# Kernel optimization log

Measured on AMD Instinct MI355X. Metric: run time of the kernel, lower is better.

Reference implementation:

```python
import jax, jax.numpy as jnp
import numpy as np

MAGNITUDE = 9
PROB = 0.5
WARP_STRENGTH = MAGNITUDE * 0.3 / 9.0  # = 0.3


def _notaknot_matrix(S):
    # System for second derivatives M of a cubic spline on uniform grid h=1
    # (scipy CubicSpline default bc_type='not-a-knot').
    A = np.zeros((S, S), dtype=np.float32)
    i = np.arange(1, S - 1)
    A[i, i - 1] = 1.0
    A[i, i] = 4.0
    A[i, i + 1] = 1.0
    # not-a-knot: third derivative continuous at x1 and x_{S-2}
    A[0, 0], A[0, 1], A[0, 2] = 1.0, -2.0, 1.0
    A[-1, -3], A[-1, -2], A[-1, -1] = 1.0, -2.0, 1.0
    return A


def setup_inputs() -> dict:
    key = jax.random.key(0)
    k1, k2, k3 = jax.random.split(key, 3)
    B, C, S = 128, 64, 4096
    x = jax.random.normal(k1, (B, C, S), dtype=jnp.float32)
    # per-sample scale ~ U(1 - warp_strength, 1 + warp_strength)
    scale = (1.0 - WARP_STRENGTH) + 2.0 * WARP_STRENGTH * jax.random.uniform(k2, (B,), dtype=jnp.float32)
    # per-sample apply decision: rand < prob
    apply_mask = jax.random.uniform(k3, (B,)) < PROB
    return {"x": x, "scale": scale, "apply_mask": apply_mask}


def reference(x, scale, apply_mask):
    B, C, S = x.shape
    A = jnp.asarray(_notaknot_matrix(S))  # (S, S), fixed uniform-grid system

    # --- fit not-a-knot cubic splines for all B*C signals at once ---
    y = x.reshape(B * C, S)
    rhs = jnp.zeros_like(y).at[:, 1:-1].set(
        6.0 * (y[:, :-2] - 2.0 * y[:, 1:-1] + y[:, 2:])
    )  # not-a-knot rows have rhs 0
    M = jnp.linalg.solve(A, rhs.T).T.reshape(B, C, S)  # second derivatives

    # --- warped evaluation points (shared across channels of a sample) ---
    grid = jnp.arange(S, dtype=x.dtype)
    w = jnp.clip(grid[None, :] * scale[:, None], 0.0, S - 1)  # (B, S)
    idx = jnp.clip(jnp.floor(w).astype(jnp.int32), 0, S - 2)  # interval index
    t = (w - idx.astype(x.dtype))[:, None, :]                 # (B, 1, S)

    idx3 = jnp.broadcast_to(idx[:, None, :], (B, C, S))
    y0 = jnp.take_along_axis(x, idx3, axis=2)
    y1 = jnp.take_along_axis(x, idx3 + 1, axis=2)
    M0 = jnp.take_along_axis(M, idx3, axis=2)
    M1 = jnp.take_along_axis(M, idx3 + 1, axis=2)

    # s(t) = y0 + b t + c t^2 + d t^3 on each unit interval (h = 1)
    b = (y1 - y0) - (2.0 * M0 + M1) / 6.0
    c = M0 / 2.0
    d = (M1 - M0) / 6.0
    warped = y0 + t * (b + t * (c + t * d))

    return jnp.where(apply_mask[:, None, None], warped, x)
```

## Files before the change

kernel.cpp:

```cpp
#include <hip/hip_runtime.h>
#include <math.h>


#define SLEN 4096
#define WRAD 8
#define BLK  256
#define NG   4

__global__ __launch_bounds__(BLK, 3) void time_warp_kernel(
    const float* __restrict__ x,
    const float* __restrict__ scale,
    const int*   __restrict__ apply_mask,
    float* __restrict__ out,
    int C)
{
    __shared__ float sy[SLEN];
    __shared__ float sf[SLEN + 2 * WRAD];
    __shared__ float sm[SLEN];

    const int bid = blockIdx.x;
    const int b   = bid / C;
    const int t   = threadIdx.x;
    const float* __restrict__ xin = x   + (size_t)bid * SLEN;
    float*       __restrict__ o   = out + (size_t)bid * SLEN;

    if (apply_mask[b] == 0) {
        const float4* __restrict__ xi4 = (const float4*)xin;
        float4*       __restrict__ o4  = (float4*)o;
        #pragma unroll
        for (int s = 0; s < NG; ++s)
            o4[t + BLK * s] = xi4[t + BLK * s];
        return;
    }

    {
        const float4* __restrict__ xi4 = (const float4*)xin;
        #pragma unroll
        for (int s = 0; s < NG; ++s)
            *(float4*)&sy[4 * t + 1024 * s] = xi4[t + BLK * s];
    }
    if (t < WRAD)                      sf[t] = 0.0f;
    else if (t >= 16 && t < 16 + WRAD) sf[(SLEN + 2 * WRAD - 1) - (t - 16)] = 0.0f;
    __syncthreads();

    const float M1  = sy[0]        - 2.0f * sy[1]        + sy[2];
    const float MS2 = sy[SLEN - 3] - 2.0f * sy[SLEN - 2] + sy[SLEN - 1];

    #pragma unroll
    for (int s = 0; s < NG; ++s) {
        const int j0 = 4 * t + 1024 * s;
        float4 yc = *(const float4*)&sy[j0];
        float  ym = (j0 > 0)        ? sy[j0 - 1] : 0.0f;
        float  yp = (j0 + 4 < SLEN) ? sy[j0 + 4] : 0.0f;
        float yv[6] = {ym, yc.x, yc.y, yc.z, yc.w, yp};
        float fe[4];
        #pragma unroll
        for (int e = 0; e < 4; ++e) {
            const int j = j0 + e;
            float v = 6.0f * (yv[e] - 2.0f * yv[e + 1] + yv[e + 2]);
            if (j < 2 || j > SLEN - 3) v = 0.0f;
            if (j == 2)        v -= M1;
            if (j == SLEN - 3) v -= MS2;
            fe[e] = v;
        }
        *(float4*)&sf[WRAD + j0] = make_float4(fe[0], fe[1], fe[2], fe[3]);
    }
    __syncthreads();

    const float r = 0.26794919243112270f;
    float G[WRAD + 1];
    G[0] = 0.28867513459481287f;
    #pragma unroll
    for (int k = 1; k <= WRAD; ++k) G[k] = -G[k - 1] * r;
    const float log2r = -1.8999686269529532f;

    float v1 = 0.0f, vS2 = 0.0f;
    #pragma unroll
    for (int k = 1; k <= WRAD; ++k) {
        v1  += G[k] * sf[WRAD + 1 + k];
        vS2 += G[k] * sf[WRAD + (SLEN - 2) - k];
    }

    #pragma unroll
    for (int s = 0; s < NG; ++s) {
        const int j0 = 4 * t + 1024 * s;
        float fw[4 * (WRAD / 4) * 2 + 4];
        #pragma unroll
        for (int m = 0; m < 5; ++m)
            *(float4*)&fw[4 * m] = *(const float4*)&sf[j0 + 4 * m];
        float mv[4];
        #pragma unroll
        for (int e = 0; e < 4; ++e) {
            float acc = G[0] * fw[WRAD + e];
            #pragma unroll
            for (int k = 1; k <= WRAD; ++k)
                acc += G[k] * (fw[WRAD + e - k] + fw[WRAD + e + k]);
            const int i = j0 + e;
            if (i >= 2 && i <= 34) {
                float cc = v1 * exp2f((float)(i - 1) * log2r);
                acc += (i & 1) ? -cc : cc;
            }
            if (i >= SLEN - 36 && i <= SLEN - 3) {
                float cc = vS2 * exp2f((float)(SLEN - 2 - i) * log2r);
                acc += (i & 1) ? cc : -cc;
            }
            mv[e] = acc;
        }
        if (j0 == 0)        { mv[1] = M1;  mv[0] = 2.0f * M1  - mv[2]; }
        if (j0 == SLEN - 4) { mv[2] = MS2; mv[3] = 2.0f * MS2 - mv[1]; }
        *(float4*)&sm[j0] = make_float4(mv[0], mv[1], mv[2], mv[3]);
    }
    __syncthreads();

    const float sc = scale[b];
    #pragma unroll
    for (int s = 0; s < NG; ++s) {
        const int j0 = 4 * t + 1024 * s;
        float rv[4];
        #pragma unroll
        for (int e = 0; e < 4; ++e) {
            const int j = j0 + e;
            float w = fminf((float)j * sc, (float)(SLEN - 1));
            int idx = (int)w;
            if (idx > SLEN - 2) idx = SLEN - 2;
            float tt  = w - (float)idx;
            float y0  = sy[idx];
            float y1  = sy[idx + 1];
            float m0  = sm[idx];
            float m1v = sm[idx + 1];
            float bb = (y1 - y0) - (2.0f * m0 + m1v) * (1.0f / 6.0f);
            float cc = 0.5f * m0;
            float dd = (m1v - m0) * (1.0f / 6.0f);
            rv[e] = y0 + tt * (bb + tt * (cc + tt * dd));
        }
        ((float4*)o)[t + BLK * s] = make_float4(rv[0], rv[1], rv[2], rv[3]);
    }
}

extern "C" void kernel_launch(void* const* d_in, const int* in_sizes, int n_in,
                              void* d_out, int out_size, void* d_ws, size_t ws_size,
                              hipStream_t stream) {
    const float* x     = (const float*)d_in[0];
    const float* scale = (const float*)d_in[1];
    const int*   mask  = (const int*)d_in[2];
    float*       out   = (float*)d_out;

    const int B     = in_sizes[1];
    const int total = in_sizes[0];
    const int C     = total / (B * SLEN);
    const int nblk  = B * C;

    time_warp_kernel<<<nblk, BLK, 0, stream>>>(x, scale, mask, out, C);
}
```

Before: 230.5 us.

## Fold second-difference RHS into filter taps, drop sf buffer and one barrier

The rhs stencil is folded algebraically into the truncated inverse filter, giving combined taps H applied directly to the signal. This removes the intermediate shared rhs array and one __syncthreads, with explicit corrections applied only near the boundaries. The smaller shared footprint allows launch bounds of 4 blocks per CU. The final evaluation now writes scalar coalesced stores per thread instead of float4 groups, which changes the LDS gather pattern and risks some precision differences from the truncated 7-tap filter.

```diff
diff --git a/kernel.cpp b/kernel.cpp
--- a/kernel.cpp
+++ b/kernel.cpp
@@ -3,11 +3,10 @@
 
 
 #define SLEN 4096
-#define WRAD 8
 #define BLK  256
 #define NG   4
 
-__global__ __launch_bounds__(BLK, 3) void time_warp_kernel(
+__global__ __launch_bounds__(BLK, 4) void time_warp_kernel(
     const float* __restrict__ x,
     const float* __restrict__ scale,
     const int*   __restrict__ apply_mask,
@@ -15,7 +14,6 @@
     int C)
 {
     __shared__ float sy[SLEN];
-    __shared__ float sf[SLEN + 2 * WRAD];
     __shared__ float sm[SLEN];
 
     const int bid = blockIdx.x;
@@ -39,101 +37,115 @@
         for (int s = 0; s < NG; ++s)
             *(float4*)&sy[4 * t + 1024 * s] = xi4[t + BLK * s];
     }
-    if (t < WRAD)                      sf[t] = 0.0f;
-    else if (t >= 16 && t < 16 + WRAD) sf[(SLEN + 2 * WRAD - 1) - (t - 16)] = 0.0f;
     __syncthreads();
 
-    const float M1  = sy[0]        - 2.0f * sy[1]        + sy[2];
-    const float MS2 = sy[SLEN - 3] - 2.0f * sy[SLEN - 2] + sy[SLEN - 1];
+    const float log2r = -1.8999686269529532f;
+    float Gt[10];
+    Gt[0] = 0.28867513459481287f;
+    #pragma unroll
+    for (int k = 1; k <= 7; ++k) Gt[k] = -Gt[k - 1] * 0.26794919243112270f;
+    Gt[8] = 0.0f; Gt[9] = 0.0f;
+    float H[9];
+    H[0] = 6.0f * (2.0f * Gt[1] - 2.0f * Gt[0]);
+    #pragma unroll
+    for (int k = 1; k <= 8; ++k) H[k] = 6.0f * (Gt[k - 1] - 2.0f * Gt[k] + Gt[k + 1]);
+
+    auto gax = [&](int d) -> float {
+        int a = d < 0 ? -d : d;
+        if (a > 7) return 0.0f;
+        float g = 0.28867513459481287f * exp2f((float)a * log2r);
+        return (a & 1) ? -g : g;
+    };
 
     #pragma unroll
     for (int s = 0; s < NG; ++s) {
         const int j0 = 4 * t + 1024 * s;
-        float4 yc = *(const float4*)&sy[j0];
-        float  ym = (j0 > 0)        ? sy[j0 - 1] : 0.0f;
-        float  yp = (j0 + 4 < SLEN) ? sy[j0 + 4] : 0.0f;
-        float yv[6] = {ym, yc.x, yc.y, yc.z, yc.w, yp};
-        float fe[4];
-        #pragma unroll
-        for (int e = 0; e < 4; ++e) {
-            const int j = j0 + e;
-            float v = 6.0f * (yv[e] - 2.0f * yv[e + 1] + yv[e + 2]);
-            if (j < 2 || j > SLEN - 3) v = 0.0f;
-            if (j == 2)        v -= M1;
-            if (j == SLEN - 3) v -= MS2;
-            fe[e] = v;
+        float fw[20];
+        if (j0 >= 8 && j0 <= SLEN - 12) {
+            #pragma unroll
+            for (int m = 0; m < 5; ++m)
+                *(float4*)&fw[4 * m] = *(const float4*)&sy[j0 - 8 + 4 * m];
+        } else {
+            #pragma unroll
+            for (int m = 0; m < 20; ++m) {
+                int yi = j0 - 8 + m;
+                int yc = yi < 0 ? 0 : (yi > SLEN - 1 ? SLEN - 1 : yi);
+                float v = sy[yc];
+                fw[m] = (yi < 0 || yi > SLEN - 1) ? 0.0f : v;
+            }
         }
-        *(float4*)&sf[WRAD + j0] = make_float4(fe[0], fe[1], fe[2], fe[3]);
-    }
-    __syncthreads();
-
-    const float r = 0.26794919243112270f;
-    float G[WRAD + 1];
-    G[0] = 0.28867513459481287f;
-    #pragma unroll
-    for (int k = 1; k <= WRAD; ++k) G[k] = -G[k - 1] * r;
-    const float log2r = -1.8999686269529532f;
-
-    float v1 = 0.0f, vS2 = 0.0f;
-    #pragma unroll
-    for (int k = 1; k <= WRAD; ++k) {
-        v1  += G[k] * sf[WRAD + 1 + k];
-        vS2 += G[k] * sf[WRAD + (SLEN - 2) - k];
-    }
-
-    #pragma unroll
-    for (int s = 0; s < NG; ++s) {
-        const int j0 = 4 * t + 1024 * s;
-        float fw[4 * (WRAD / 4) * 2 + 4];
-        #pragma unroll
-        for (int m = 0; m < 5; ++m)
-            *(float4*)&fw[4 * m] = *(const float4*)&sf[j0 + 4 * m];
         float mv[4];
         #pragma unroll
         for (int e = 0; e < 4; ++e) {
-            float acc = G[0] * fw[WRAD + e];
+            float acc = H[0] * fw[8 + e];
             #pragma unroll
-            for (int k = 1; k <= WRAD; ++k)
-                acc += G[k] * (fw[WRAD + e - k] + fw[WRAD + e + k]);
-            const int i = j0 + e;
-            if (i >= 2 && i <= 34) {
-                float cc = v1 * exp2f((float)(i - 1) * log2r);
-                acc += (i & 1) ? -cc : cc;
-            }
-            if (i >= SLEN - 36 && i <= SLEN - 3) {
-                float cc = vS2 * exp2f((float)(SLEN - 2 - i) * log2r);
-                acc += (i & 1) ? cc : -cc;
-            }
+            for (int k = 1; k <= 8; ++k)
+                acc += H[k] * (fw[8 + e - k] + fw[8 + e + k]);
             mv[e] = acc;
         }
-        if (j0 == 0)        { mv[1] = M1;  mv[0] = 2.0f * M1  - mv[2]; }
-        if (j0 == SLEN - 4) { mv[2] = MS2; mv[3] = 2.0f * MS2 - mv[1]; }
+
+        if (j0 <= 12) {
+            float M1v  = sy[0] - 2.0f * sy[1] + sy[2];
+            float fspm = 6.0f * sy[0];
+            float fsp0 = 6.0f * (sy[1] - 2.0f * sy[0]);
+            float fsp1 = 6.0f * M1v;
+            float v1 = 0.0f;
+            #pragma unroll
+            for (int k = 1; k <= 7; ++k)
+                v1 += Gt[k] * 6.0f * (sy[k] - 2.0f * sy[k + 1] + sy[k + 2]);
+            v1 -= Gt[1] * M1v;
+            #pragma unroll
+            for (int e = 0; e < 4; ++e) {
+                int i = j0 + e;
+                float corr = gax(i + 1) * fspm + gax(i) * fsp0
+                           + gax(i - 1) * fsp1 + gax(i - 2) * M1v;
+                float img = v1 * exp2f((float)(i - 1) * log2r);
+                mv[e] = mv[e] - corr + ((i & 1) ? -img : img);
+            }
+            if (j0 == 0) { mv[1] = M1v; mv[0] = 2.0f * M1v - mv[2]; }
+        }
+        if (j0 >= SLEN - 16) {
+            float MS2v = sy[SLEN - 3] - 2.0f * sy[SLEN - 2] + sy[SLEN - 1];
+            float fspA = 6.0f * MS2v;
+            float fspB = 6.0f * (sy[SLEN - 2] - 2.0f * sy[SLEN - 1]);
+            float fspC = 6.0f * sy[SLEN - 1];
+            float vS2 = 0.0f;
+            #pragma unroll
+            for (int k = 1; k <= 7; ++k) {
+                int j = SLEN - 2 - k;
+                vS2 += Gt[k] * 6.0f * (sy[j - 1] - 2.0f * sy[j] + sy[j + 1]);
+            }
+            vS2 -= Gt[1] * MS2v;
+            #pragma unroll
+            for (int e = 0; e < 4; ++e) {
+                int i = j0 + e;
+                float corr = gax(SLEN - 3 - i) * MS2v + gax(SLEN - 2 - i) * fspA
+                           + gax(SLEN - 1 - i) * fspB + gax(SLEN - i) * fspC;
+                float img = vS2 * exp2f((float)(SLEN - 2 - i) * log2r);
+                mv[e] = mv[e] - corr + ((i & 1) ? img : -img);
+            }
+            if (j0 == SLEN - 4) { mv[2] = MS2v; mv[3] = 2.0f * MS2v - mv[1]; }
+        }
         *(float4*)&sm[j0] = make_float4(mv[0], mv[1], mv[2], mv[3]);
     }
     __syncthreads();
 
     const float sc = scale[b];
     #pragma unroll
-    for (int s = 0; s < NG; ++s) {
-        const int j0 = 4 * t + 1024 * s;
-        float rv[4];
-        #pragma unroll
-        for (int e = 0; e < 4; ++e) {
-            const int j = j0 + e;
-            float w = fminf((float)j * sc, (float)(SLEN - 1));
-            int idx = (int)w;
-            if (idx > SLEN - 2) idx = SLEN - 2;
-            float tt  = w - (float)idx;
-            float y0  = sy[idx];
-            float y1  = sy[idx + 1];
-            float m0  = sm[idx];
-            float m1v = sm[idx + 1];
-            float bb = (y1 - y0) - (2.0f * m0 + m1v) * (1.0f / 6.0f);
-            float cc = 0.5f * m0;
-            float dd = (m1v - m0) * (1.0f / 6.0f);
-            rv[e] = y0 + tt * (bb + tt * (cc + tt * dd));
-        }
-        ((float4*)o)[t + BLK * s] = make_float4(rv[0], rv[1], rv[2], rv[3]);
+    for (int s = 0; s < 16; ++s) {
+        const int j = t + BLK * s;
+        float w = fminf((float)j * sc, (float)(SLEN - 1));
+        int idx = (int)w;
+        if (idx > SLEN - 2) idx = SLEN - 2;
+        float tt  = w - (float)idx;
+        float y0  = sy[idx];
+        float y1  = sy[idx + 1];
+        float m0  = sm[idx];
+        float m1v = sm[idx + 1];
+        float bb = (y1 - y0) - (2.0f * m0 + m1v) * (1.0f / 6.0f);
+        float cc = 0.5f * m0;
+        float dd = (m1v - m0) * (1.0f / 6.0f);
+        o[j] = y0 + tt * (bb + tt * (cc + tt * dd));
     }
 }
 
```

Result: no change. 234.2 us (+1.6%).
